# Kernel optimization log

Measured on AMD Instinct MI355X. Metric: run time of the kernel, lower is better.

## Reference

```python
import jax, jax.numpy as jnp
import numpy as np

N = 50000          # nodes
E = 800000         # edges
F_IN = 128         # node_features
HID = 128          # hidden_dim
OUT = 64           # out_channels
TOP = 4            # top_features (gate channels)
EXP = 3            # experts
G = 64             # num graphs in batch
TEMP = 101.0       # 100 - 0/(200*0.01) + final_temperature(1.0) at batch counter 0


def setup_inputs() -> dict:
    key = jax.random.key(0)
    ks = jax.random.split(key, 12)
    s = 0.08  # weight init scale
    x = jax.random.normal(ks[0], (N, F_IN), jnp.float32)
    top_features = jax.random.normal(ks[1], (N, TOP), jnp.float32)
    edge_index = jax.random.randint(ks[2], (2, E), 0, N, dtype=jnp.int64)
    batch = jnp.sort(jax.random.randint(ks[3], (N,), 0, G, dtype=jnp.int64))
    W0 = jax.random.normal(ks[4], (EXP, F_IN, HID), jnp.float32) * s
    b0 = jax.random.normal(ks[5], (EXP, HID), jnp.float32) * s
    Wg0 = jax.random.normal(ks[6], (EXP, TOP), jnp.float32) * s
    W1 = jax.random.normal(ks[7], (EXP, HID, HID), jnp.float32) * s
    b1 = jax.random.normal(ks[8], (EXP, HID), jnp.float32) * s
    Wg1 = jax.random.normal(ks[9], (EXP, TOP), jnp.float32) * s
    Wf = jax.random.normal(ks[10], (HID, OUT), jnp.float32) * s
    bf = jax.random.normal(ks[11], (OUT,), jnp.float32) * s
    return {"x": x, "top_features": top_features, "edge_index": edge_index,
            "batch": batch, "W0": W0, "b0": b0, "Wg0": Wg0,
            "W1": W1, "b1": b1, "Wg1": Wg1, "Wf": Wf, "bf": bf}


def reference(x, top_features, edge_index, batch, W0, b0, Wg0, W1, b1, Wg1, Wf, bf):
    # GCN with self-loops and symmetric normalization (PyG GCNConv default)
    sl = jnp.arange(N, dtype=edge_index.dtype)
    src = jnp.concatenate([edge_index[0], sl])
    dst = jnp.concatenate([edge_index[1], sl])
    deg = jax.ops.segment_sum(jnp.ones_like(src, jnp.float32), dst, num_segments=N)
    dinv = jax.lax.rsqrt(deg)  # deg >= 1 thanks to self loops
    norm = dinv[src] * dinv[dst]  # [E+N]

    def camoe_layer(h, W, b, Wg):
        # gate: softmax over experts at temperature TEMP
        gate = jax.nn.softmax((top_features @ Wg.T) / TEMP, axis=-1)  # [N, EXP]
        out = jnp.zeros((N, W.shape[2]), h.dtype)
        for e in range(EXP):  # small fixed expert loop (keeps peak memory low)
            he = h @ W[e]                                            # [N, HID]
            agg = jax.ops.segment_sum(he[src] * norm[:, None], dst, num_segments=N)
            out = out + gate[:, e:e + 1] * jax.nn.relu(agg + b[e])
        return out

    h = camoe_layer(x, W0, b0, Wg0)
    # F.dropout before last layer: eval mode -> identity
    h = camoe_layer(h, W1, b1, Wg1)

    # global mean pool over graphs
    sums = jax.ops.segment_sum(h, batch, num_segments=G)             # [G, HID]
    cnt = jax.ops.segment_sum(jnp.ones((N,), h.dtype), batch, num_segments=G)
    pooled = sums / jnp.maximum(cnt, 1.0)[:, None]
    return pooled @ Wf + bf                                          # [G, OUT]
```

## Files before the change

### kernel.cpp

```cpp
#include <hip/hip_runtime.h>
#include <hip/hip_bf16.h>

#define HID 128
#define EXP 3
#define TOP 4
#define OUTC 64
#define SLOTC 64

typedef __bf16 bf16x8 __attribute__((ext_vector_type(8)));
typedef float f32x16 __attribute__((ext_vector_type(16)));
typedef float f32x2 __attribute__((ext_vector_type(2)));

#define GLDS_STRIDE 272
#define OUT_STRIDE 132

__device__ __forceinline__ unsigned int pack4_fp8(float a, float b, float c, float d) {
    int v = 0;
    v = __builtin_amdgcn_cvt_pk_fp8_f32(a, b, v, false);
    v = __builtin_amdgcn_cvt_pk_fp8_f32(c, d, v, true);
    return (unsigned int)v;
}

__device__ __forceinline__ void unpack4_fp8(unsigned int v, float* out) {
    f32x2 lo = __builtin_amdgcn_cvt_pk_f32_fp8((int)v, false);
    f32x2 hi = __builtin_amdgcn_cvt_pk_f32_fp8((int)v, true);
    out[0] = lo[0]; out[1] = lo[1]; out[2] = hi[0]; out[3] = hi[1];
}

__device__ __forceinline__ void fma16_fp8(uint4 a, float w, float* acc) {
    unsigned int q[4] = {a.x, a.y, a.z, a.w};
#pragma unroll
    for (int k = 0; k < 4; ++k) {
        float f[4];
        unpack4_fp8(q[k], f);
#pragma unroll
        for (int j = 0; j < 4; ++j) acc[k * 4 + j] += f[j] * w;
    }
}


__global__ __launch_bounds__(256) void mega0_kernel(
        const int* __restrict__ src, const int* __restrict__ dst,
        int* __restrict__ cnt, int* __restrict__ slots, int E,
        const float* __restrict__ x, unsigned int* __restrict__ x8,
        const float* __restrict__ tf, const float* __restrict__ Wg0,
        const float* __restrict__ Wg1, float* __restrict__ gates,
        const int* __restrict__ batch, int* __restrict__ gstart,
        const float* __restrict__ W0, const float* __restrict__ W1,
        __bf16* __restrict__ ph0, __bf16* __restrict__ ph1,
        int N, int G, int nFill, int nConv, int nGate) {
    int b = blockIdx.x;
    int t = threadIdx.x;

    if (b < nFill) {
        int slice = b & 7;
        int base = (b >> 3) * 2048 + t * 8;
        if (base < E) {
            if (base + 8 <= E) {
                int4 d0 = *(const int4*)(dst + base);
                int4 d1 = *(const int4*)(dst + base + 4);
                int dv[8] = {d0.x, d0.y, d0.z, d0.w, d1.x, d1.y, d1.z, d1.w};
#pragma unroll
                for (int k = 0; k < 8; ++k) {
                    int d = dv[k];
                    if (((d >> 6) & 7) != slice) continue;
                    int s = src[base + k];
                    int p = atomicAdd(&cnt[d], 1);
                    if (p < SLOTC) slots[(size_t)d * SLOTC + p] = s;
                }
            } else {
                for (int i = base; i < E; ++i) {
                    int d = dst[i];
                    if (((d >> 6) & 7) != slice) continue;
                    int s = src[i];
                    int p = atomicAdd(&cnt[d], 1);
                    if (p < SLOTC) slots[(size_t)d * SLOTC + p] = s;
                }
            }
        }
        return;
    }
    b -= nFill;
    if (b < nConv) {
        int i = b * 256 + t;
        int total16 = N * (HID / 16);
        if (i < total16) {
            const float4* xp = (const float4*)x + (size_t)i * 4;
            float4 v0 = xp[0], v1 = xp[1], v2 = xp[2], v3 = xp[3];
            uint4 o;
            o.x = pack4_fp8(v0.x, v0.y, v0.z, v0.w);
            o.y = pack4_fp8(v1.x, v1.y, v1.z, v1.w);
            o.z = pack4_fp8(v2.x, v2.y, v2.z, v2.w);
            o.w = pack4_fp8(v3.x, v3.y, v3.z, v3.w);
            ((uint4*)x8)[i] = o;
        }
        return;
    }
    b -= nConv;
    if (b < nGate) {
        int n = b * 256 + t;
        if (n >= N) return;
        float4 tv = *(const float4*)(tf + (size_t)n * TOP);
        const float* Wg[2] = {Wg0, Wg1};
#pragma unroll
        for (int l = 0; l < 2; ++l) {
            float lg[EXP];
#pragma unroll
            for (int e = 0; e < EXP; ++e) {
                const float* w = Wg[l] + e * TOP;
                lg[e] = (tv.x * w[0] + tv.y * w[1] + tv.z * w[2] + tv.w * w[3]) * (1.0f / 101.0f);
            }
            float m = fmaxf(lg[0], fmaxf(lg[1], lg[2]));
            float e0 = expf(lg[0] - m), e1 = expf(lg[1] - m), e2 = expf(lg[2] - m);
            float inv = 1.0f / (e0 + e1 + e2);
            gates[n * 6 + l * 3 + 0] = e0 * inv;
            gates[n * 6 + l * 3 + 1] = e1 * inv;
            gates[n * 6 + l * 3 + 2] = e2 * inv;
        }
        return;
    }
    b -= nGate;
    if (b == 0) {
        int g = t;
        if (g > G) return;
        if (g == G) { gstart[G] = N; return; }
        int lo = 0, hi = N;
        while (lo < hi) {
            int mid = (lo + hi) >> 1;
            if (batch[mid] < g) lo = mid + 1; else hi = mid;
        }
        gstart[g] = lo;
        return;
    }
    b -= 1;
    int job = b * 4 + (t >> 6);
    if (job >= 192) return;
    int l = t & 63;
    int layer = job / 96;
    int rem = job % 96;
    int e = rem / 32;
    int s = (rem % 32) / 4;
    int c = rem % 4;
    const float* W = layer ? W1 : W0;
    __bf16* ph = layer ? ph1 : ph0;
    size_t dstbase = (size_t)((((e * 8 + s) * 4 + c) * 64 + l)) * 8;
    int kbase = s * 16 + (l >> 5) * 8;
    int ncol = c * 32 + (l & 31);
#pragma unroll
    for (int j = 0; j < 8; ++j) {
        float w = W[(size_t)e * (HID * HID) + (size_t)(kbase + j) * HID + ncol];
        ph[dstbase + j] = (__bf16)w;
    }
}


__global__ __launch_bounds__(512, 4) void fused_layer_kernel(
        const unsigned char* __restrict__ h8in,
        const __bf16* __restrict__ wpkh,
        const float* __restrict__ bias, const float* __restrict__ gates, int gate_off,
        const int* __restrict__ cnt, const int* __restrict__ slots,
        unsigned char* __restrict__ hout8,
        const int* __restrict__ batch, float* __restrict__ pooled, int N) {
    __shared__ char lds[64 * OUT_STRIDE * 4];
    int tid = threadIdx.x;
    int row0 = blockIdx.x * 64;

    {
        int r = tid >> 3;
        int part = tid & 7;
        int n = row0 + r;
        float acc[16];
#pragma unroll
        for (int j = 0; j < 16; ++j) acc[j] = 0.f;
        if (n < N) {
            const unsigned char* hb = h8in + part * 16;
            int degt = cnt[n];
            int deg = min(degt, SLOTC);
            float dn = rsqrtf((float)degt + 1.0f);
            uint4 v = *(const uint4*)(hb + (size_t)n * HID);
            float ws = dn * dn;
            {
                unsigned int q[4] = {v.x, v.y, v.z, v.w};
#pragma unroll
                for (int k = 0; k < 4; ++k) {
                    float f[4];
                    unpack4_fp8(q[k], f);
#pragma unroll
                    for (int j = 0; j < 4; ++j) acc[k * 4 + j] = f[j] * ws;
                }
            }
            const int* sl = slots + (size_t)n * SLOTC;
            int i = 0;
            for (; i + 4 <= deg; i += 4) {
                int4 sv = *(const int4*)(sl + i);
                int s0 = sv.x, s1 = sv.y, s2 = sv.z, s3 = sv.w;
                int c0 = cnt[s0], c1 = cnt[s1], c2 = cnt[s2], c3 = cnt[s3];
                uint4 a0 = *(const uint4*)(hb + (size_t)s0 * HID);
                uint4 a1 = *(const uint4*)(hb + (size_t)s1 * HID);
                uint4 a2 = *(const uint4*)(hb + (size_t)s2 * HID);
                uint4 a3 = *(const uint4*)(hb + (size_t)s3 * HID);
                float w0 = rsqrtf((float)c0 + 1.0f) * dn;
                float w1 = rsqrtf((float)c1 + 1.0f) * dn;
                float w2 = rsqrtf((float)c2 + 1.0f) * dn;
                float w3 = rsqrtf((float)c3 + 1.0f) * dn;
                fma16_fp8(a0, w0, acc);
                fma16_fp8(a1, w1, acc);
                fma16_fp8(a2, w2, acc);
                fma16_fp8(a3, w3, acc);
            }
            for (; i < deg; ++i) {
                int s0 = sl[i];
                float w0 = rsqrtf((float)cnt[s0] + 1.0f) * dn;
                uint4 a0 = *(const uint4*)(hb + (size_t)s0 * HID);
                fma16_fp8(a0, w0, acc);
            }
        }
        char* drow = lds + r * GLDS_STRIDE + part * 32;
        bf16x8 h0, h1;
#pragma unroll
        for (int j = 0; j < 8; ++j) { h0[j] = (__bf16)acc[j]; h1[j] = (__bf16)acc[8 + j]; }
        *(bf16x8*)drow = h0;
        *(bf16x8*)(drow + 16) = h1;
    }
    __syncthreads();

    int lane = tid & 63;
    int wave = tid >> 6;
    int m = lane & 31;
    int g = lane >> 5;
    int rhalf = wave & 1;
    int cq = wave >> 1;
    const char* arow = lds + (rhalf * 32 + m) * GLDS_STRIDE + g * 16;
    int rowbase = row0 + rhalf * 32 + 4 * g;

    float F[16];
#pragma unroll
    for (int r = 0; r < 16; ++r) F[r] = 0.f;

    for (int e = 0; e < EXP; ++e) {
        f32x16 acc;
#pragma unroll
        for (int r = 0; r < 16; ++r) acc[r] = 0.f;

#pragma unroll
        for (int s = 0; s < 8; ++s) {
            bf16x8 Ah = *(const bf16x8*)(arow + s * 32);
            bf16x8 Bh = *(const bf16x8*)(wpkh + (size_t)(((e * 8 + s) * 4 + cq) * 64 + lane) * 8);
            acc = __builtin_amdgcn_mfma_f32_32x32x16_bf16(Ah, Bh, acc, 0, 0, 0);
        }
        float gt[16];
#pragma unroll
        for (int r = 0; r < 16; ++r) {
            int rr = rowbase + (r & 3) + 8 * (r >> 2);
            gt[r] = (rr < N) ? gates[(size_t)rr * 6 + gate_off + e] : 0.f;
        }
        float bb = bias[e * HID + cq * 32 + m];
#pragma unroll
        for (int r = 0; r < 16; ++r)
            F[r] += gt[r] * fmaxf(acc[r] + bb, 0.f);
    }

    __syncthreads();
    float* lds32 = (float*)lds;
    {
        int colg = cq * 32 + m;
#pragma unroll
        for (int r = 0; r < 16; ++r) {
            int lr = rhalf * 32 + 4 * g + (r & 3) + 8 * (r >> 2);
            lds32[lr * OUT_STRIDE + colg] = F[r];
        }
    }
    __syncthreads();

    if (hout8) {
#pragma unroll
        for (int it = 0; it < 4; ++it) {
            int id = tid + it * 512;
            int r = id >> 5;
            int c4 = id & 31;
            int gr = row0 + r;
            if (gr < N) {
                const float* src = &lds32[r * OUT_STRIDE + c4 * 4];
                *(unsigned int*)(hout8 + (size_t)gr * HID + c4 * 4) =
                    pack4_fp8(src[0], src[1], src[2], src[3]);
            }
        }
    }
    if (pooled) {
        int col = tid & 127;
        int rbase = (tid >> 7) * 16;
        int cur = -1;
        float acc = 0.f;
        for (int r = 0; r < 16; ++r) {
            int gr = row0 + rbase + r;
            if (gr >= N) break;
            int gb = batch[gr];
            if (gb != cur) {
                if (cur >= 0) atomicAdd(&pooled[cur * HID + col], acc);
                acc = 0.f;
                cur = gb;
            }
            acc += lds32[(rbase + r) * OUT_STRIDE + col];
        }
        if (cur >= 0) atomicAdd(&pooled[cur * HID + col], acc);
    }
}


__global__ __launch_bounds__(64) void final_kernel(const float* __restrict__ pooled,
                                                   const int* __restrict__ gstart,
                                                   const float* __restrict__ Wf,
                                                   const float* __restrict__ bf,
                                                   float* __restrict__ out) {
    __shared__ float ps[HID];
    int g = blockIdx.x;
    int o = threadIdx.x;
    float invc = 1.0f / fmaxf((float)(gstart[g + 1] - gstart[g]), 1.0f);
    ps[o] = pooled[g * HID + o] * invc;
    ps[o + 64] = pooled[g * HID + o + 64] * invc;
    __syncthreads();
    float acc = bf[o];
#pragma unroll 8
    for (int k = 0; k < HID; ++k) acc = fmaf(ps[k], Wf[k * OUTC + o], acc);
    out[g * OUTC + o] = acc;
}


extern "C" void kernel_launch(void* const* d_in, const int* in_sizes, int n_in,
                              void* d_out, int out_size, void* d_ws, size_t ws_size,
                              hipStream_t stream) {
    const float* x   = (const float*)d_in[0];
    const float* tf  = (const float*)d_in[1];
    const int*   ei  = (const int*)d_in[2];
    const int*   bat = (const int*)d_in[3];
    const float* W0  = (const float*)d_in[4];
    const float* b0  = (const float*)d_in[5];
    const float* Wg0 = (const float*)d_in[6];
    const float* W1  = (const float*)d_in[7];
    const float* b1  = (const float*)d_in[8];
    const float* Wg1 = (const float*)d_in[9];
    const float* Wf  = (const float*)d_in[10];
    const float* bf  = (const float*)d_in[11];
    float* out = (float*)d_out;

    const int N = in_sizes[0] / HID;
    const int E = in_sizes[2] / 2;
    const int G = out_size / OUTC;

    char* p = (char*)d_ws;
    auto alloc = [&](size_t bytes) -> void* {
        void* r = (void*)p;
        p += (bytes + 255) & ~(size_t)255;
        return r;
    };
    int*           cnt    = (int*)alloc((size_t)N * 4);
    float*         pooled = (float*)alloc((size_t)G * HID * 4);
    int*           slots  = (int*)alloc((size_t)N * SLOTC * 4);
    float*         gates  = (float*)alloc((size_t)N * 6 * 4);
    unsigned char* x8     = (unsigned char*)alloc((size_t)N * HID);
    unsigned char* h8b    = (unsigned char*)alloc((size_t)N * HID);
    int*           gstart = (int*)alloc((size_t)(G + 1) * 4);
    __bf16*        wpkh0  = (__bf16*)alloc((size_t)EXP * HID * HID * 2);
    __bf16*        wpkh1  = (__bf16*)alloc((size_t)EXP * HID * HID * 2);

    const int* src = ei;
    const int* dst = ei + E;

    size_t zlen = (size_t)((char*)pooled - (char*)cnt) + (size_t)G * HID * 4;
    hipMemsetAsync(cnt, 0, zlen, stream);

    const int nFill = ((E + 2047) / 2048) * 8;
    const int nConv = (N * (HID / 16) + 255) / 256;
    const int nGate = (N + 255) / 256;
    const int megaBlocks = nFill + nConv + nGate + 1 + 48;

    mega0_kernel<<<megaBlocks, 256, 0, stream>>>(src, dst, cnt, slots, E,
                                                 x, (unsigned int*)x8,
                                                 tf, Wg0, Wg1, gates,
                                                 bat, gstart,
                                                 W0, W1, wpkh0, wpkh1,
                                                 N, G, nFill, nConv, nGate);

    int gemm_blocks = (N + 63) / 64;

    fused_layer_kernel<<<gemm_blocks, 512, 0, stream>>>(x8, wpkh0, b0, gates, 0,
                                                        cnt, slots,
                                                        h8b, nullptr, nullptr, N);
    fused_layer_kernel<<<gemm_blocks, 512, 0, stream>>>(h8b, wpkh1, b1, gates, 3,
                                                        cnt, slots,
                                                        nullptr, bat, pooled, N);

    final_kernel<<<G, 64, 0, stream>>>(pooled, gstart, Wf, bf, out);
}
```

Measured before the change: 218.1 us.

## Pre-scale node features by source degree norm to drop per-edge rsqrt gathers

Factors the symmetric GCN normalization so each node's features are pre-multiplied by its own dinv before the fp8 conversion, and the layer output is likewise pre-scaled by dinv before being stored. Aggregation becomes a plain sum of neighbor rows followed by one multiply by the destination dinv. This removes the per-edge random gather of cnt[src] and its rsqrt. The x conversion now has to run in a separate kernel after the degree counts are complete, which adds a launch and takes it out of the overlapped mega kernel. Quantizing pre-scaled values to fp8 also slightly changes numerical behavior.

```diff
diff --git a/kernel.cpp b/kernel.cpp
--- a/kernel.cpp
+++ b/kernel.cpp
@@ -27,14 +27,14 @@
     out[0] = lo[0]; out[1] = lo[1]; out[2] = hi[0]; out[3] = hi[1];
 }
 
-__device__ __forceinline__ void fma16_fp8(uint4 a, float w, float* acc) {
+__device__ __forceinline__ void add16_fp8(uint4 a, float* acc) {
     unsigned int q[4] = {a.x, a.y, a.z, a.w};
 #pragma unroll
     for (int k = 0; k < 4; ++k) {
         float f[4];
         unpack4_fp8(q[k], f);
 #pragma unroll
-        for (int j = 0; j < 4; ++j) acc[k * 4 + j] += f[j] * w;
+        for (int j = 0; j < 4; ++j) acc[k * 4 + j] += f[j];
     }
 }
 
@@ -42,13 +42,12 @@
 __global__ __launch_bounds__(256) void mega0_kernel(
         const int* __restrict__ src, const int* __restrict__ dst,
         int* __restrict__ cnt, int* __restrict__ slots, int E,
-        const float* __restrict__ x, unsigned int* __restrict__ x8,
         const float* __restrict__ tf, const float* __restrict__ Wg0,
         const float* __restrict__ Wg1, float* __restrict__ gates,
         const int* __restrict__ batch, int* __restrict__ gstart,
         const float* __restrict__ W0, const float* __restrict__ W1,
         __bf16* __restrict__ ph0, __bf16* __restrict__ ph1,
-        int N, int G, int nFill, int nConv, int nGate) {
+        int N, int G, int nFill, int nGate) {
     int b = blockIdx.x;
     int t = threadIdx.x;
 
@@ -81,22 +80,6 @@
         return;
     }
     b -= nFill;
-    if (b < nConv) {
-        int i = b * 256 + t;
-        int total16 = N * (HID / 16);
-        if (i < total16) {
-            const float4* xp = (const float4*)x + (size_t)i * 4;
-            float4 v0 = xp[0], v1 = xp[1], v2 = xp[2], v3 = xp[3];
-            uint4 o;
-            o.x = pack4_fp8(v0.x, v0.y, v0.z, v0.w);
-            o.y = pack4_fp8(v1.x, v1.y, v1.z, v1.w);
-            o.z = pack4_fp8(v2.x, v2.y, v2.z, v2.w);
-            o.w = pack4_fp8(v3.x, v3.y, v3.z, v3.w);
-            ((uint4*)x8)[i] = o;
-        }
-        return;
-    }
-    b -= nConv;
     if (b < nGate) {
         int n = b * 256 + t;
         if (n >= N) return;
@@ -154,6 +137,25 @@
 }
 
 
+__global__ __launch_bounds__(256) void prep2_kernel(const float* __restrict__ x,
+                                                    unsigned int* __restrict__ x8,
+                                                    const int* __restrict__ cnt, int N) {
+    int i = blockIdx.x * 256 + threadIdx.x;
+    int total16 = N * (HID / 16);
+    if (i >= total16) return;
+    int n = i >> 3;
+    float dn = rsqrtf((float)cnt[n] + 1.0f);
+    const float4* xp = (const float4*)x + (size_t)i * 4;
+    float4 v0 = xp[0], v1 = xp[1], v2 = xp[2], v3 = xp[3];
+    uint4 o;
+    o.x = pack4_fp8(v0.x * dn, v0.y * dn, v0.z * dn, v0.w * dn);
+    o.y = pack4_fp8(v1.x * dn, v1.y * dn, v1.z * dn, v1.w * dn);
+    o.z = pack4_fp8(v2.x * dn, v2.y * dn, v2.z * dn, v2.w * dn);
+    o.w = pack4_fp8(v3.x * dn, v3.y * dn, v3.z * dn, v3.w * dn);
+    ((uint4*)x8)[i] = o;
+}
+
+
 __global__ __launch_bounds__(512, 4) void fused_layer_kernel(
         const unsigned char* __restrict__ h8in,
         const __bf16* __restrict__ wpkh,
@@ -178,7 +180,6 @@
             int deg = min(degt, SLOTC);
             float dn = rsqrtf((float)degt + 1.0f);
             uint4 v = *(const uint4*)(hb + (size_t)n * HID);
-            float ws = dn * dn;
             {
                 unsigned int q[4] = {v.x, v.y, v.z, v.w};
 #pragma unroll
@@ -186,34 +187,28 @@
                     float f[4];
                     unpack4_fp8(q[k], f);
 #pragma unroll
-                    for (int j = 0; j < 4; ++j) acc[k * 4 + j] = f[j] * ws;
+                    for (int j = 0; j < 4; ++j) acc[k * 4 + j] = f[j];
                 }
             }
             const int* sl = slots + (size_t)n * SLOTC;
             int i = 0;
             for (; i + 4 <= deg; i += 4) {
                 int4 sv = *(const int4*)(sl + i);
-                int s0 = sv.x, s1 = sv.y, s2 = sv.z, s3 = sv.w;
-                int c0 = cnt[s0], c1 = cnt[s1], c2 = cnt[s2], c3 = cnt[s3];
-                uint4 a0 = *(const uint4*)(hb + (size_t)s0 * HID);
-                uint4 a1 = *(const uint4*)(hb + (size_t)s1 * HID);
-                uint4 a2 = *(const uint4*)(hb + (size_t)s2 * HID);
-                uint4 a3 = *(const uint4*)(hb + (size_t)s3 * HID);
-                float w0 = rsqrtf((float)c0 + 1.0f) * dn;
-                float w1 = rsqrtf((float)c1 + 1.0f) * dn;
-                float w2 = rsqrtf((float)c2 + 1.0f) * dn;
-                float w3 = rsqrtf((float)c3 + 1.0f) * dn;
-                fma16_fp8(a0, w0, acc);
-                fma16_fp8(a1, w1, acc);
-                fma16_fp8(a2, w2, acc);
-                fma16_fp8(a3, w3, acc);
+                uint4 a0 = *(const uint4*)(hb + (size_t)sv.x * HID);
+                uint4 a1 = *(const uint4*)(hb + (size_t)sv.y * HID);
+                uint4 a2 = *(const uint4*)(hb + (size_t)sv.z * HID);
+                uint4 a3 = *(const uint4*)(hb + (size_t)sv.w * HID);
+                add16_fp8(a0, acc);
+                add16_fp8(a1, acc);
+                add16_fp8(a2, acc);
+                add16_fp8(a3, acc);
             }
             for (; i < deg; ++i) {
-                int s0 = sl[i];
-                float w0 = rsqrtf((float)cnt[s0] + 1.0f) * dn;
-                uint4 a0 = *(const uint4*)(hb + (size_t)s0 * HID);
-                fma16_fp8(a0, w0, acc);
-            }
+                uint4 a0 = *(const uint4*)(hb + (size_t)sl[i] * HID);
+                add16_fp8(a0, acc);
+            }
+#pragma unroll
+            for (int j = 0; j < 16; ++j) acc[j] *= dn;
         }
         char* drow = lds + r * GLDS_STRIDE + part * 32;
         bf16x8 h0, h1;
@@ -280,9 +275,10 @@
             int c4 = id & 31;
             int gr = row0 + r;
             if (gr < N) {
+                float dr = rsqrtf((float)cnt[gr] + 1.0f);
                 const float* src = &lds32[r * OUT_STRIDE + c4 * 4];
                 *(unsigned int*)(hout8 + (size_t)gr * HID + c4 * 4) =
-                    pack4_fp8(src[0], src[1], src[2], src[3]);
+                    pack4_fp8(src[0] * dr, src[1] * dr, src[2] * dr, src[3] * dr);
             }
         }
     }
@@ -370,16 +366,17 @@
     hipMemsetAsync(cnt, 0, zlen, stream);
 
     const int nFill = ((E + 2047) / 2048) * 8;
-    const int nConv = (N * (HID / 16) + 255) / 256;
     const int nGate = (N + 255) / 256;
-    const int megaBlocks = nFill + nConv + nGate + 1 + 48;
+    const int megaBlocks = nFill + nGate + 1 + 48;
 
     mega0_kernel<<<megaBlocks, 256, 0, stream>>>(src, dst, cnt, slots, E,
-                                                 x, (unsigned int*)x8,
                                                  tf, Wg0, Wg1, gates,
                                                  bat, gstart,
                                                  W0, W1, wpkh0, wpkh1,
-                                                 N, G, nFill, nConv, nGate);
+                                                 N, G, nFill, nGate);
+
+    const int prepBlocks = (N * (HID / 16) + 255) / 256;
+    prep2_kernel<<<prepBlocks, 256, 0, stream>>>(x, (unsigned int*)x8, cnt, N);
 
     int gemm_blocks = (N + 63) / 64;
 
```

Result: no change. 221.1 us (+1.4%).
